# Kernel tuning notes

Measured on AMD Instinct MI355X. Metric: run time of the kernel, lower is better.

The kernel has to match this reference:

```python
import jax, jax.numpy as jnp
import numpy as np

DIM = 1024

def setup_inputs() -> dict:
    key = jax.random.key(0)
    ks = jax.random.split(key, 7)
    s = 1.0 / np.sqrt(DIM)
    x = jax.random.normal(ks[0], (8, 2048, DIM), dtype=jnp.float32)
    Wq = jax.random.uniform(ks[1], (DIM, DIM), jnp.float32, -s, s)
    bq = jax.random.uniform(ks[2], (DIM,), jnp.float32, -s, s)
    Wk = jax.random.uniform(ks[3], (DIM, DIM), jnp.float32, -s, s)
    bk = jax.random.uniform(ks[4], (DIM,), jnp.float32, -s, s)
    Wv = jax.random.uniform(ks[5], (DIM, DIM), jnp.float32, -s, s)
    bv = jax.random.uniform(ks[6], (DIM,), jnp.float32, -s, s)
    return {"x": x, "Wq": Wq, "bq": bq, "Wk": Wk, "bk": bk, "Wv": Wv, "bv": bv}

def reference(x, Wq, bq, Wk, bk, Wv, bv):
    # nn.Linear: y = x @ W.T + b
    q = jnp.einsum('bsd,ed->bse', x, Wq) + bq  # [B,S,D]
    k = jnp.einsum('bsd,ed->bse', x, Wk) + bk
    v = jnp.einsum('bsd,ed->bse', x, Wv) + bv
    scores = jnp.einsum('bqd,bkd->bqk', q, k) / jnp.sqrt(jnp.float32(DIM))
    attn = jax.nn.softmax(scores, axis=-1)
    return jnp.einsum('bqk,bkd->bqd', attn, v)
```

## Files before the change

kernel.cpp:

```cpp
#include <hip/hip_runtime.h>

#define DIM 1024
#define SEQ 2048

typedef __attribute__((ext_vector_type(8))) short bf16x8;
typedef __attribute__((ext_vector_type(16))) float f32x16;
typedef __attribute__((ext_vector_type(4))) unsigned short us4;
typedef __attribute__((ext_vector_type(4))) _Float16 h4;

__device__ __forceinline__ unsigned short f2bf(float f) {
    union { float f; unsigned int u; } v; v.f = f;
    unsigned int r = (v.u + 0x7FFFu + ((v.u >> 16) & 1u)) >> 16;
    return (unsigned short)r;
}

#define GLOAD(gp, lp) __builtin_amdgcn_global_load_lds( \
    (const __attribute__((address_space(1))) unsigned int*)(gp), \
    (__attribute__((address_space(3))) unsigned int*)(lp), 16, 0, 0)

#define MFMA32(a, b, c) __builtin_amdgcn_mfma_f32_32x32x16_bf16((a), (b), (c), 0, 0, 0)

__global__ __launch_bounds__(256) void cast_f32_bf16(const float* __restrict__ src,
                                                     unsigned short* __restrict__ dst, int n) {
    int i = (blockIdx.x * 256 + threadIdx.x) * 8;
    if (i >= n) return;
    float4 a = *(const float4*)(src + i);
    float4 b = *(const float4*)(src + i + 4);
    us4 lo = { f2bf(a.x), f2bf(a.y), f2bf(a.z), f2bf(a.w) };
    us4 hi = { f2bf(b.x), f2bf(b.y), f2bf(b.z), f2bf(b.w) };
    *(us4*)(dst + i) = lo;
    *(us4*)(dst + i + 4) = hi;
}

__device__ __forceinline__ void gemm128_core(
    const unsigned short* __restrict__ A, const unsigned short* __restrict__ B,
    int lda, int ldb, int K, char* smem, f32x16 acc[2][2])
{
    const int tid = threadIdx.x;
    const int lane = tid & 63;
    const int wm = (tid >> 6) >> 1;
    const int wn = (tid >> 6) & 1;
    const int l31 = lane & 31, lhi = lane >> 5;

    const int schunk = ((tid & 3) ^ ((tid >> 3) & 3)) * 8;
    const unsigned short* paw = A + (size_t)(tid >> 2) * lda + schunk;
    const unsigned short* pbw = B + (size_t)(tid >> 2) * ldb + schunk;
    const int doff = tid * 16;

    const int fsw = (l31 >> 1) & 3;
    const int abase = (wm * 64 + l31) * 64;
    const int bbase = 8192 + (wn * 64 + l31) * 64;
    int csw[4];
#pragma unroll
    for (int c = 0; c < 4; c++) csw[c] = (c ^ fsw) * 16;

    const int NT = K >> 5;

#define STAGE128(bb, kt) do { \
    GLOAD(paw + (kt),                     smem + (bb) + doff); \
    GLOAD(paw + (kt) + (size_t)64 * lda,  smem + (bb) + 4096 + doff); \
    GLOAD(pbw + (kt),                     smem + (bb) + 8192 + doff); \
    GLOAD(pbw + (kt) + (size_t)64 * ldb,  smem + (bb) + 12288 + doff); \
} while (0)

    STAGE128(0, 0);

    for (int T = 0; T < NT; ++T) {
        asm volatile("s_waitcnt vmcnt(0)" ::: "memory");
        __builtin_amdgcn_s_barrier();

        if (T + 1 < NT) STAGE128(((T + 1) & 1) * 16384, (size_t)(T + 1) * 32);

        const char* db = smem + (T & 1) * 16384;
        bf16x8 a0[2], a1[2], b0[2], b1[2];
#pragma unroll
        for (int mi = 0; mi < 2; mi++) {
            a0[mi] = *(const bf16x8*)(db + abase + mi * 2048 + csw[lhi]);
            a1[mi] = *(const bf16x8*)(db + abase + mi * 2048 + csw[2 + lhi]);
        }
#pragma unroll
        for (int nj = 0; nj < 2; nj++) {
            b0[nj] = *(const bf16x8*)(db + bbase + nj * 2048 + csw[lhi]);
            b1[nj] = *(const bf16x8*)(db + bbase + nj * 2048 + csw[2 + lhi]);
        }

        __builtin_amdgcn_s_setprio(1);
#pragma unroll
        for (int mi = 0; mi < 2; mi++)
#pragma unroll
            for (int nj = 0; nj < 2; nj++)
                acc[mi][nj] = MFMA32(a0[mi], b0[nj], acc[mi][nj]);
#pragma unroll
        for (int mi = 0; mi < 2; mi++)
#pragma unroll
            for (int nj = 0; nj < 2; nj++)
                acc[mi][nj] = MFMA32(a1[mi], b1[nj], acc[mi][nj]);
        __builtin_amdgcn_s_setprio(0);
    }
#undef STAGE128
}

#define ACC_INIT() \
    f32x16 acc[2][2]; \
    _Pragma("unroll") for (int i = 0; i < 2; i++) \
    _Pragma("unroll") for (int jj = 0; jj < 2; jj++) acc[i][jj] = (f32x16){}; \


__global__ __launch_bounds__(256) void gemm_qkv(
    const unsigned short* __restrict__ xb, const unsigned short* __restrict__ wb,
    const float* __restrict__ bq, const float* __restrict__ bk, const float* __restrict__ bv,
    unsigned short* __restrict__ qb, unsigned short* __restrict__ kb, unsigned short* __restrict__ vt)
{
    __shared__ char smem[32768];
    const int bid = blockIdx.x;
    const int lb = (bid & 7) * 384 + (bid >> 3);
    const int bz = lb >> 10;
    const int r0 = lb & 1023;
    const int m0 = (r0 >> 3) * 128, n0 = (r0 & 7) * 128;
    const float* bias = (bz == 0) ? bq : ((bz == 1) ? bk : bv);
    ACC_INIT();
    gemm128_core(xb + (size_t)m0 * DIM, wb + (size_t)bz * DIM * DIM + (size_t)n0 * DIM,
                 DIM, DIM, DIM, smem, acc);
    const int lane = threadIdx.x & 63, wid = threadIdx.x >> 6;
    const int wm = wid >> 1, wn = wid & 1;
    const int l31 = lane & 31, lhi = lane >> 5;
#pragma unroll
    for (int mi = 0; mi < 2; mi++)
#pragma unroll
        for (int nj = 0; nj < 2; nj++) {
            const int col = n0 + wn * 64 + nj * 32 + l31;
            const float bcol = bias[col];
            if (bz < 2) {
                unsigned short* C = (bz == 0) ? qb : kb;
                const float scale = (bz == 0) ? 0.03125f : 1.0f;
#pragma unroll
                for (int r = 0; r < 16; r++) {
                    const int row = m0 + wm * 64 + mi * 32 + (r & 3) + 8 * (r >> 2) + 4 * lhi;
                    C[(size_t)row * DIM + col] = f2bf((acc[mi][nj][r] + bcol) * scale);
                }
            } else {
#pragma unroll
                for (int r4 = 0; r4 < 4; r4++) {
                    const int s0 = m0 + wm * 64 + mi * 32 + 8 * r4 + 4 * lhi;
                    const int b = s0 >> 11, s = s0 & 2047;
                    us4 pk = { f2bf(acc[mi][nj][r4 * 4] + bcol),
                               f2bf(acc[mi][nj][r4 * 4 + 1] + bcol),
                               f2bf(acc[mi][nj][r4 * 4 + 2] + bcol),
                               f2bf(acc[mi][nj][r4 * 4 + 3] + bcol) };
                    *(us4*)&vt[((size_t)b << 21) + ((size_t)col << 11) + s] = pk;
                }
            }
        }
}

__global__ __launch_bounds__(256) void gemm_qk(
    const unsigned short* __restrict__ qb, const unsigned short* __restrict__ kb,
    unsigned short* __restrict__ sb)
{
    __shared__ char smem[32768];
    const int bid = blockIdx.x;
    const int lb = (bid & 7) * 256 + (bid >> 3);
    const int b = lb >> 8;
    const int r0 = lb & 255;
    const int m0 = (r0 >> 4) * 128, n0 = (r0 & 15) * 128;
    ACC_INIT();
    gemm128_core(qb + ((size_t)b * SEQ + m0) * DIM, kb + ((size_t)b * SEQ + n0) * DIM,
                 DIM, DIM, DIM, smem, acc);
    const int lane = threadIdx.x & 63, wid = threadIdx.x >> 6;
    const int wm = wid >> 1, wn = wid & 1;
    const int l31 = lane & 31, lhi = lane >> 5;
    _Float16* sh = (_Float16*)sb + (size_t)b * SEQ * SEQ;
#pragma unroll
    for (int mi = 0; mi < 2; mi++)
#pragma unroll
        for (int nj = 0; nj < 2; nj++) {
            const int col = n0 + wn * 64 + nj * 32 + l31;
#pragma unroll
            for (int r = 0; r < 16; r++) {
                const int row = m0 + wm * 64 + mi * 32 + (r & 3) + 8 * (r >> 2) + 4 * lhi;
                sh[(size_t)row * SEQ + col] = (_Float16)acc[mi][nj][r];
            }
        }
}

__global__ __launch_bounds__(256) void softmax_p(unsigned short* __restrict__ sb)
{
    const int lane = threadIdx.x & 63, wid = threadIdx.x >> 6;
    const size_t row = (size_t)blockIdx.x * 4 + wid;
    unsigned short* rp = sb + row * SEQ;
    float v[32];
#pragma unroll
    for (int j = 0; j < 8; j++) {
        h4 h = *(const h4*)(rp + (j * 64 + lane) * 4);
#pragma unroll
        for (int e = 0; e < 4; e++) v[j * 4 + e] = (float)h[e];
    }
    float m = -1e30f;
#pragma unroll
    for (int i = 0; i < 32; i++) m = fmaxf(m, v[i]);
#pragma unroll
    for (int msk = 1; msk <= 32; msk <<= 1) m = fmaxf(m, __shfl_xor(m, msk, 64));
    float s = 0.f;
#pragma unroll
    for (int i = 0; i < 32; i++) { v[i] = __expf(v[i] - m); s += v[i]; }
#pragma unroll
    for (int msk = 1; msk <= 32; msk <<= 1) s += __shfl_xor(s, msk, 64);
    float inv = 1.0f / s;
#pragma unroll
    for (int j = 0; j < 8; j++) {
        us4 pu = { f2bf(v[j * 4] * inv), f2bf(v[j * 4 + 1] * inv),
                   f2bf(v[j * 4 + 2] * inv), f2bf(v[j * 4 + 3] * inv) };
        *(us4*)(rp + (j * 64 + lane) * 4) = pu;
    }
}

__global__ __launch_bounds__(256) void gemm_pv(
    const unsigned short* __restrict__ pb, const unsigned short* __restrict__ vt,
    float* __restrict__ out)
{
    __shared__ char smem[32768];
    const int bid = blockIdx.x;
    const int lb = (bid & 7) * 128 + (bid >> 3);
    const int b = lb >> 7;
    const int r0 = lb & 127;
    const int m0 = (r0 >> 3) * 128, n0 = (r0 & 7) * 128;
    ACC_INIT();
    gemm128_core(pb + ((size_t)b * SEQ + m0) * SEQ, vt + ((size_t)b * DIM + n0) * SEQ,
                 SEQ, SEQ, SEQ, smem, acc);
    const int lane = threadIdx.x & 63, wid = threadIdx.x >> 6;
    const int wm = wid >> 1, wn = wid & 1;
    const int l31 = lane & 31, lhi = lane >> 5;
    float* O = out + (size_t)b * SEQ * DIM;
#pragma unroll
    for (int mi = 0; mi < 2; mi++)
#pragma unroll
        for (int nj = 0; nj < 2; nj++) {
            const int col = n0 + wn * 64 + nj * 32 + l31;
#pragma unroll
            for (int r = 0; r < 16; r++) {
                const int row = m0 + wm * 64 + mi * 32 + (r & 3) + 8 * (r >> 2) + 4 * lhi;
                O[(size_t)row * DIM + col] = acc[mi][nj][r];
            }
        }
}

extern "C" void kernel_launch(void* const* d_in, const int* in_sizes, int n_in,
                              void* d_out, int out_size, void* d_ws, size_t ws_size,
                              hipStream_t stream) {
    const float* x  = (const float*)d_in[0];
    const float* Wq = (const float*)d_in[1];
    const float* bq = (const float*)d_in[2];
    const float* Wk = (const float*)d_in[3];
    const float* bk = (const float*)d_in[4];
    const float* Wv = (const float*)d_in[5];
    const float* bv = (const float*)d_in[6];
    float* out = (float*)d_out;
    char* ws = (char*)d_ws;

    unsigned short* xb = (unsigned short*)(ws);
    unsigned short* wb = (unsigned short*)(ws + 33554432);
    unsigned short* qb = (unsigned short*)(ws + 39845888);
    unsigned short* kb = (unsigned short*)(ws + 73400320);
    unsigned short* vt = (unsigned short*)(ws + 106954752);
    unsigned short* sb = (unsigned short*)(ws + 140509184);

    cast_f32_bf16<<<dim3(8192), 256, 0, stream>>>(x, xb, 16777216);
    cast_f32_bf16<<<dim3(512), 256, 0, stream>>>(Wq, wb, 1048576);
    cast_f32_bf16<<<dim3(512), 256, 0, stream>>>(Wk, wb + 1048576, 1048576);
    cast_f32_bf16<<<dim3(512), 256, 0, stream>>>(Wv, wb + 2097152, 1048576);

    gemm_qkv<<<dim3(3072), 256, 0, stream>>>(xb, wb, bq, bk, bv, qb, kb, vt);
    gemm_qk<<<dim3(2048), 256, 0, stream>>>(qb, kb, sb);
    softmax_p<<<dim3(4096), 256, 0, stream>>>(sb);
    gemm_pv<<<dim3(1024), 256, 0, stream>>>(sb, vt, out);
}
```

Baseline: 351.3 us.

## Switch GEMMs to 128x256 tiles with B operands loaded directly to registers

Replaces the 128x128 shared-memory GEMM core with a 128x256 tile where each of four waves owns a 64-column strip. Only the A tile is staged through LDS (double-buffered); each wave loads its B fragments straight from global memory into registers, prefetched one k-step ahead. Grids are halved accordingly, and launch bounds request two blocks per CU. The aim is to raise arithmetic intensity and cut LDS traffic and footprint, at the cost of more accumulator registers and uncoalesced per-lane global B loads that can stall the MFMA pipeline.

```diff
diff --git a/kernel.cpp b/kernel.cpp
--- a/kernel.cpp
+++ b/kernel.cpp
@@ -32,100 +32,104 @@
     *(us4*)(dst + i + 4) = hi;
 }
 
-__device__ __forceinline__ void gemm128_core(
+__device__ __forceinline__ void gemm128x256_core(
     const unsigned short* __restrict__ A, const unsigned short* __restrict__ B,
-    int lda, int ldb, int K, char* smem, f32x16 acc[2][2])
+    int lda, int ldb, int K, char* smem, f32x16 acc[4][2])
 {
     const int tid = threadIdx.x;
     const int lane = tid & 63;
-    const int wm = (tid >> 6) >> 1;
-    const int wn = (tid >> 6) & 1;
+    const int wn = tid >> 6;
     const int l31 = lane & 31, lhi = lane >> 5;
 
     const int schunk = ((tid & 3) ^ ((tid >> 3) & 3)) * 8;
     const unsigned short* paw = A + (size_t)(tid >> 2) * lda + schunk;
-    const unsigned short* pbw = B + (size_t)(tid >> 2) * ldb + schunk;
     const int doff = tid * 16;
 
     const int fsw = (l31 >> 1) & 3;
-    const int abase = (wm * 64 + l31) * 64;
-    const int bbase = 8192 + (wn * 64 + l31) * 64;
     int csw[4];
 #pragma unroll
     for (int c = 0; c < 4; c++) csw[c] = (c ^ fsw) * 16;
+    const int ab0 = l31 * 64;
+
+    const unsigned short* pb = B + (size_t)(wn * 64 + l31) * ldb + lhi * 8;
+    const size_t bnj = (size_t)32 * ldb;
 
     const int NT = K >> 5;
 
-#define STAGE128(bb, kt) do { \
+#define SA(bb, kt) do { \
     GLOAD(paw + (kt),                     smem + (bb) + doff); \
     GLOAD(paw + (kt) + (size_t)64 * lda,  smem + (bb) + 4096 + doff); \
-    GLOAD(pbw + (kt),                     smem + (bb) + 8192 + doff); \
-    GLOAD(pbw + (kt) + (size_t)64 * ldb,  smem + (bb) + 12288 + doff); \
 } while (0)
-
-    STAGE128(0, 0);
-
-    for (int T = 0; T < NT; ++T) {
-        asm volatile("s_waitcnt vmcnt(0)" ::: "memory");
-        __builtin_amdgcn_s_barrier();
-
-        if (T + 1 < NT) STAGE128(((T + 1) & 1) * 16384, (size_t)(T + 1) * 32);
-
-        const char* db = smem + (T & 1) * 16384;
-        bf16x8 a0[2], a1[2], b0[2], b1[2];
-#pragma unroll
-        for (int mi = 0; mi < 2; mi++) {
-            a0[mi] = *(const bf16x8*)(db + abase + mi * 2048 + csw[lhi]);
-            a1[mi] = *(const bf16x8*)(db + abase + mi * 2048 + csw[2 + lhi]);
-        }
-#pragma unroll
-        for (int nj = 0; nj < 2; nj++) {
-            b0[nj] = *(const bf16x8*)(db + bbase + nj * 2048 + csw[lhi]);
-            b1[nj] = *(const bf16x8*)(db + bbase + nj * 2048 + csw[2 + lhi]);
-        }
-
-        __builtin_amdgcn_s_setprio(1);
-#pragma unroll
-        for (int mi = 0; mi < 2; mi++)
-#pragma unroll
-            for (int nj = 0; nj < 2; nj++)
-                acc[mi][nj] = MFMA32(a0[mi], b0[nj], acc[mi][nj]);
-#pragma unroll
-        for (int mi = 0; mi < 2; mi++)
-#pragma unroll
-            for (int nj = 0; nj < 2; nj++)
-                acc[mi][nj] = MFMA32(a1[mi], b1[nj], acc[mi][nj]);
-        __builtin_amdgcn_s_setprio(0);
+#define LB(dst, kt) do { \
+    dst[0][0] = *(const bf16x8*)(pb + (kt)); \
+    dst[0][1] = *(const bf16x8*)(pb + (kt) + 16); \
+    dst[1][0] = *(const bf16x8*)(pb + bnj + (kt)); \
+    dst[1][1] = *(const bf16x8*)(pb + bnj + (kt) + 16); \
+} while (0)
+#define TILE(bufoff, bcur) do { \
+    bf16x8 a[4][2]; \
+    _Pragma("unroll") \
+    for (int mi = 0; mi < 4; mi++) { \
+        a[mi][0] = *(const bf16x8*)(smem + (bufoff) + ab0 + mi * 2048 + csw[lhi]); \
+        a[mi][1] = *(const bf16x8*)(smem + (bufoff) + ab0 + mi * 2048 + csw[2 + lhi]); \
+    } \
+    __builtin_amdgcn_s_setprio(1); \
+    _Pragma("unroll") \
+    for (int ks = 0; ks < 2; ks++) \
+        _Pragma("unroll") \
+        for (int mi = 0; mi < 4; mi++) \
+            _Pragma("unroll") \
+            for (int nj = 0; nj < 2; nj++) \
+                acc[mi][nj] = MFMA32(a[mi][ks], bcur[nj][ks], acc[mi][nj]); \
+    __builtin_amdgcn_s_setprio(0); \
+    asm volatile("s_waitcnt vmcnt(0)" ::: "memory"); \
+    __builtin_amdgcn_s_barrier(); \
+} while (0)
+
+    bf16x8 bA[2][2], bB[2][2];
+    SA(0, 0);
+    LB(bA, 0);
+    asm volatile("s_waitcnt vmcnt(0)" ::: "memory");
+    __builtin_amdgcn_s_barrier();
+
+    for (int T = 0; T < NT; T += 2) {
+        if (T + 1 < NT) { SA(8192, (T + 1) * 32); LB(bB, (T + 1) * 32); }
+        TILE(0, bA);
+        if (T + 1 < NT) {
+            if (T + 2 < NT) { SA(0, (T + 2) * 32); LB(bA, (T + 2) * 32); }
+            TILE(8192, bB);
+        }
     }
-#undef STAGE128
+#undef SA
+#undef LB
+#undef TILE
 }
 
 #define ACC_INIT() \
-    f32x16 acc[2][2]; \
-    _Pragma("unroll") for (int i = 0; i < 2; i++) \
+    f32x16 acc[4][2]; \
+    _Pragma("unroll") for (int i = 0; i < 4; i++) \
     _Pragma("unroll") for (int jj = 0; jj < 2; jj++) acc[i][jj] = (f32x16){}; \
 
 
-__global__ __launch_bounds__(256) void gemm_qkv(
+__global__ __launch_bounds__(256, 2) void gemm_qkv(
     const unsigned short* __restrict__ xb, const unsigned short* __restrict__ wb,
     const float* __restrict__ bq, const float* __restrict__ bk, const float* __restrict__ bv,
     unsigned short* __restrict__ qb, unsigned short* __restrict__ kb, unsigned short* __restrict__ vt)
 {
-    __shared__ char smem[32768];
+    __shared__ char smem[16384];
     const int bid = blockIdx.x;
-    const int lb = (bid & 7) * 384 + (bid >> 3);
-    const int bz = lb >> 10;
-    const int r0 = lb & 1023;
-    const int m0 = (r0 >> 3) * 128, n0 = (r0 & 7) * 128;
+    const int lb = (bid & 7) * 192 + (bid >> 3);
+    const int bz = lb >> 9;
+    const int r0 = lb & 511;
+    const int m0 = (r0 >> 2) * 128, n0 = (r0 & 3) * 256;
     const float* bias = (bz == 0) ? bq : ((bz == 1) ? bk : bv);
     ACC_INIT();
-    gemm128_core(xb + (size_t)m0 * DIM, wb + (size_t)bz * DIM * DIM + (size_t)n0 * DIM,
-                 DIM, DIM, DIM, smem, acc);
-    const int lane = threadIdx.x & 63, wid = threadIdx.x >> 6;
-    const int wm = wid >> 1, wn = wid & 1;
-    const int l31 = lane & 31, lhi = lane >> 5;
-#pragma unroll
-    for (int mi = 0; mi < 2; mi++)
+    gemm128x256_core(xb + (size_t)m0 * DIM, wb + (size_t)bz * DIM * DIM + (size_t)n0 * DIM,
+                     DIM, DIM, DIM, smem, acc);
+    const int lane = threadIdx.x & 63, wn = threadIdx.x >> 6;
+    const int l31 = lane & 31, lhi = lane >> 5;
+#pragma unroll
+    for (int mi = 0; mi < 4; mi++)
 #pragma unroll
         for (int nj = 0; nj < 2; nj++) {
             const int col = n0 + wn * 64 + nj * 32 + l31;
@@ -135,13 +139,13 @@
                 const float scale = (bz == 0) ? 0.03125f : 1.0f;
 #pragma unroll
                 for (int r = 0; r < 16; r++) {
-                    const int row = m0 + wm * 64 + mi * 32 + (r & 3) + 8 * (r >> 2) + 4 * lhi;
+                    const int row = m0 + mi * 32 + (r & 3) + 8 * (r >> 2) + 4 * lhi;
                     C[(size_t)row * DIM + col] = f2bf((acc[mi][nj][r] + bcol) * scale);
                 }
             } else {
 #pragma unroll
                 for (int r4 = 0; r4 < 4; r4++) {
-                    const int s0 = m0 + wm * 64 + mi * 32 + 8 * r4 + 4 * lhi;
+                    const int s0 = m0 + mi * 32 + 8 * r4 + 4 * lhi;
                     const int b = s0 >> 11, s = s0 & 2047;
                     us4 pk = { f2bf(acc[mi][nj][r4 * 4] + bcol),
                                f2bf(acc[mi][nj][r4 * 4 + 1] + bcol),
@@ -153,31 +157,30 @@
         }
 }
 
-__global__ __launch_bounds__(256) void gemm_qk(
+__global__ __launch_bounds__(256, 2) void gemm_qk(
     const unsigned short* __restrict__ qb, const unsigned short* __restrict__ kb,
     unsigned short* __restrict__ sb)
 {
-    __shared__ char smem[32768];
+    __shared__ char smem[16384];
     const int bid = blockIdx.x;
-    const int lb = (bid & 7) * 256 + (bid >> 3);
-    const int b = lb >> 8;
-    const int r0 = lb & 255;
-    const int m0 = (r0 >> 4) * 128, n0 = (r0 & 15) * 128;
+    const int lb = (bid & 7) * 128 + (bid >> 3);
+    const int b = lb >> 7;
+    const int r0 = lb & 127;
+    const int m0 = (r0 >> 3) * 128, n0 = (r0 & 7) * 256;
     ACC_INIT();
-    gemm128_core(qb + ((size_t)b * SEQ + m0) * DIM, kb + ((size_t)b * SEQ + n0) * DIM,
-                 DIM, DIM, DIM, smem, acc);
-    const int lane = threadIdx.x & 63, wid = threadIdx.x >> 6;
-    const int wm = wid >> 1, wn = wid & 1;
+    gemm128x256_core(qb + ((size_t)b * SEQ + m0) * DIM, kb + ((size_t)b * SEQ + n0) * DIM,
+                     DIM, DIM, DIM, smem, acc);
+    const int lane = threadIdx.x & 63, wn = threadIdx.x >> 6;
     const int l31 = lane & 31, lhi = lane >> 5;
     _Float16* sh = (_Float16*)sb + (size_t)b * SEQ * SEQ;
 #pragma unroll
-    for (int mi = 0; mi < 2; mi++)
+    for (int mi = 0; mi < 4; mi++)
 #pragma unroll
         for (int nj = 0; nj < 2; nj++) {
             const int col = n0 + wn * 64 + nj * 32 + l31;
 #pragma unroll
             for (int r = 0; r < 16; r++) {
-                const int row = m0 + wm * 64 + mi * 32 + (r & 3) + 8 * (r >> 2) + 4 * lhi;
+                const int row = m0 + mi * 32 + (r & 3) + 8 * (r >> 2) + 4 * lhi;
                 sh[(size_t)row * SEQ + col] = (_Float16)acc[mi][nj][r];
             }
         }
@@ -214,31 +217,30 @@
     }
 }
 
-__global__ __launch_bounds__(256) void gemm_pv(
+__global__ __launch_bounds__(256, 2) void gemm_pv(
     const unsigned short* __restrict__ pb, const unsigned short* __restrict__ vt,
     float* __restrict__ out)
 {
-    __shared__ char smem[32768];
+    __shared__ char smem[16384];
     const int bid = blockIdx.x;
-    const int lb = (bid & 7) * 128 + (bid >> 3);
-    const int b = lb >> 7;
-    const int r0 = lb & 127;
-    const int m0 = (r0 >> 3) * 128, n0 = (r0 & 7) * 128;
+    const int lb = (bid & 7) * 64 + (bid >> 3);
+    const int b = lb >> 6;
+    const int r0 = lb & 63;
+    const int m0 = (r0 >> 2) * 128, n0 = (r0 & 3) * 256;
     ACC_INIT();
-    gemm128_core(pb + ((size_t)b * SEQ + m0) * SEQ, vt + ((size_t)b * DIM + n0) * SEQ,
-                 SEQ, SEQ, SEQ, smem, acc);
-    const int lane = threadIdx.x & 63, wid = threadIdx.x >> 6;
-    const int wm = wid >> 1, wn = wid & 1;
+    gemm128x256_core(pb + ((size_t)b * SEQ + m0) * SEQ, vt + ((size_t)b * DIM + n0) * SEQ,
+                     SEQ, SEQ, SEQ, smem, acc);
+    const int lane = threadIdx.x & 63, wn = threadIdx.x >> 6;
     const int l31 = lane & 31, lhi = lane >> 5;
     float* O = out + (size_t)b * SEQ * DIM;
 #pragma unroll
-    for (int mi = 0; mi < 2; mi++)
+    for (int mi = 0; mi < 4; mi++)
 #pragma unroll
         for (int nj = 0; nj < 2; nj++) {
             const int col = n0 + wn * 64 + nj * 32 + l31;
 #pragma unroll
             for (int r = 0; r < 16; r++) {
-                const int row = m0 + wm * 64 + mi * 32 + (r & 3) + 8 * (r >> 2) + 4 * lhi;
+                const int row = m0 + mi * 32 + (r & 3) + 8 * (r >> 2) + 4 * lhi;
                 O[(size_t)row * DIM + col] = acc[mi][nj][r];
             }
         }
@@ -269,8 +271,8 @@
     cast_f32_bf16<<<dim3(512), 256, 0, stream>>>(Wk, wb + 1048576, 1048576);
     cast_f32_bf16<<<dim3(512), 256, 0, stream>>>(Wv, wb + 2097152, 1048576);
 
-    gemm_qkv<<<dim3(3072), 256, 0, stream>>>(xb, wb, bq, bk, bv, qb, kb, vt);
-    gemm_qk<<<dim3(2048), 256, 0, stream>>>(qb, kb, sb);
+    gemm_qkv<<<dim3(1536), 256, 0, stream>>>(xb, wb, bq, bk, bv, qb, kb, vt);
+    gemm_qk<<<dim3(1024), 256, 0, stream>>>(qb, kb, sb);
     softmax_p<<<dim3(4096), 256, 0, stream>>>(sb);
-    gemm_pv<<<dim3(1024), 256, 0, stream>>>(sb, vt, out);
-}
+    gemm_pv<<<dim3(512), 256, 0, stream>>>(sb, vt, out);
+}
```

Result: slower. 363.4 us, median of 2 (+3.4%).
